# Kernel optimization log

Hardware: AMD Instinct MI355X
Metric: run time of the kernel (lower is better)

The kernel has to match this reference:

```python
import jax, jax.numpy as jnp
import numpy as np

B, S, D, F, E, K = 4, 2048, 512, 2048, 8, 2


def setup_inputs() -> dict:
    key = jax.random.key(0)
    kx, kg, kw, kv, k2 = jax.random.split(key, 5)
    scale = 0.02
    return {
        "x": jax.random.normal(kx, (B, S, D), dtype=jnp.float32),
        "Wg": jax.random.normal(kg, (D, E), dtype=jnp.float32) * scale,
        "W": jax.random.normal(kw, (E, D, F), dtype=jnp.float32) * scale,
        "V": jax.random.normal(kv, (E, D, F), dtype=jnp.float32) * scale,
        "W2": jax.random.normal(k2, (E, F, D), dtype=jnp.float32) * scale,
    }


def reference(x, Wg, W, V, W2):
    # Gating: top-k over expert logits, softmax over the selected k logits.
    gate_logits = jnp.einsum("bsd,de->bse", x, Wg)                 # [B,S,E]
    topv, topi = jax.lax.top_k(gate_logits, K)                      # [B,S,K]
    w = jax.nn.softmax(topv, axis=-1)                               # [B,S,K]
    # Dense per-token combine weights: gw[b,s,e] = sum_k w[b,s,k]*[topi[b,s,k]==e]
    gw = jnp.sum(w[..., None] * jax.nn.one_hot(topi, E, dtype=x.dtype), axis=-2)  # [B,S,E]

    y = jnp.zeros_like(x)
    n_experts = W.shape[0]
    for e in range(n_experts):  # fixed small loop over experts
        h = jax.nn.silu(jnp.einsum("bsd,df->bsf", x, W[e])) * jnp.einsum("bsd,df->bsf", x, V[e])
        y = y + gw[..., e:e + 1] * jnp.einsum("bsf,fd->bsd", h, W2[e])
    return y
```

## Files before the change

### kernel.cpp

```cpp
#include <hip/hip_runtime.h>
#include <hip/hip_bf16.h>
#include <stdint.h>

#define TT 8192
#define DD 512
#define FF 2048
#define EE 8
#define MAXT 136

typedef __attribute__((ext_vector_type(8))) short bf16x8;
typedef __attribute__((ext_vector_type(4))) float f32x4;

static __device__ __forceinline__ unsigned short f2b(float f) {
  union { __hip_bfloat16 b; unsigned short u; } cv;
  cv.b = __float2bfloat16(f);
  return cv.u;
}

static __device__ __forceinline__ void gload16(const void* g, void* l) {
  __builtin_amdgcn_global_load_lds(
      (const __attribute__((address_space(1))) unsigned int*)g,
      (__attribute__((address_space(3))) unsigned int*)l, 16, 0, 0);
}

#define VMCNT12 asm volatile("s_waitcnt vmcnt(12)" ::: "memory")
#define VMCNT6  asm volatile("s_waitcnt vmcnt(6)" ::: "memory")
#define VMCNT0  asm volatile("s_waitcnt vmcnt(0)" ::: "memory")
#define BARX    asm volatile("s_barrier" ::: "memory")

__launch_bounds__(256)
__global__ void k_prep(const float* __restrict__ x, const float* __restrict__ Wg,
                       unsigned short* __restrict__ xb,
                       int* __restrict__ te, float* __restrict__ tw) {
  int wid = threadIdx.x >> 6, lane = threadIdx.x & 63;
  int t = blockIdx.x * 4 + wid;
  const float* xr = x + (size_t)t * DD;
  unsigned short* xbr = xb + (size_t)t * DD;
  int d0 = lane * 8;

  float4 v0 = *(const float4*)(xr + d0);
  float4 v1 = *(const float4*)(xr + d0 + 4);
  ushort4 o0, o1;
  o0.x = f2b(v0.x); o0.y = f2b(v0.y); o0.z = f2b(v0.z); o0.w = f2b(v0.w);
  o1.x = f2b(v1.x); o1.y = f2b(v1.y); o1.z = f2b(v1.z); o1.w = f2b(v1.w);
  *(ushort4*)(xbr + d0) = o0;
  *(ushort4*)(xbr + d0 + 4) = o1;

  float xv[8] = {v0.x, v0.y, v0.z, v0.w, v1.x, v1.y, v1.z, v1.w};
  float acc[EE];
#pragma unroll
  for (int e = 0; e < EE; e++) acc[e] = 0.f;
#pragma unroll
  for (int j = 0; j < 8; j++) {
    const float* wg = Wg + (size_t)(d0 + j) * EE;
    float4 a = *(const float4*)wg;
    float4 b = *(const float4*)(wg + 4);
    acc[0] += xv[j] * a.x; acc[1] += xv[j] * a.y; acc[2] += xv[j] * a.z; acc[3] += xv[j] * a.w;
    acc[4] += xv[j] * b.x; acc[5] += xv[j] * b.y; acc[6] += xv[j] * b.z; acc[7] += xv[j] * b.w;
  }
#pragma unroll
  for (int e = 0; e < EE; e++)
    for (int o = 32; o; o >>= 1) acc[e] += __shfl_xor(acc[e], o);
  if (lane == 0) {
    int e1 = 0; float v1m = acc[0];
#pragma unroll
    for (int e = 1; e < EE; e++) if (acc[e] > v1m) { v1m = acc[e]; e1 = e; }
    int e2 = -1; float v2m = -INFINITY;
#pragma unroll
    for (int e = 0; e < EE; e++) if (e != e1 && acc[e] > v2m) { v2m = acc[e]; e2 = e; }
    float ex = __expf(v2m - v1m);
    float w1 = 1.f / (1.f + ex);
    float w2 = ex / (1.f + ex);
    te[t * 2] = e1; te[t * 2 + 1] = e2;
    tw[t * 2] = w1; tw[t * 2 + 1] = w2;
  }
}

__global__ void k_tcvt_all(const float* __restrict__ W, const float* __restrict__ V,
                           const float* __restrict__ W2, unsigned short* __restrict__ Wt,
                           unsigned short* __restrict__ Vt, unsigned short* __restrict__ W2t) {
  __shared__ float tile[32][33];
  int z = blockIdx.y;
  const float* src; unsigned short* dst; int N, nbx;
  if (z < 16) {
    int e = z & 7;
    size_t base = (size_t)e * DD * FF;
    src = (z < 8 ? W : V) + base;
    dst = (z < 8 ? Wt : Vt) + base;
    N = FF; nbx = FF / 32;
  } else {
    int e = z - 16;
    size_t base = (size_t)e * DD * FF;
    src = W2 + base; dst = W2t + base;
    N = DD; nbx = DD / 32;
  }
  int M = (z < 16) ? DD : FF;
  int bx = blockIdx.x;
  int cb = (bx % nbx) * 32, rb = (bx / nbx) * 32;
  int tx = threadIdx.x, ty = threadIdx.y;
#pragma unroll
  for (int i = 0; i < 4; i++)
    tile[ty + i * 8][tx] = src[(size_t)(rb + ty + i * 8) * N + cb + tx];
  __syncthreads();
#pragma unroll
  for (int i = 0; i < 4; i++)
    dst[(size_t)(cb + ty + i * 8) * M + rb + tx] = f2b(tile[tx][ty + i * 8]);
}

__launch_bounds__(1024)
__global__ void k_route(const int* __restrict__ te, const float* __restrict__ tw,
                        int* __restrict__ ctrl, int* __restrict__ perm,
                        float* __restrict__ pw, int* __restrict__ tileE,
                        int* __restrict__ tileRow, int* __restrict__ inv) {
  __shared__ int wsum[17][EE];
  __shared__ int ebase[EE];
  int tid = threadIdx.x;
  int lane = tid & 63, wid = tid >> 6;
  int myte[16]; float mytw[16];
  int c[EE];
#pragma unroll
  for (int e = 0; e < EE; e++) c[e] = 0;
  int s0 = tid * 16;
#pragma unroll
  for (int j = 0; j < 16; j++) {
    myte[j] = te[s0 + j];
    mytw[j] = tw[s0 + j];
#pragma unroll
    for (int e = 0; e < EE; e++) if (myte[j] == e) c[e]++;
  }
  int incl[EE];
#pragma unroll
  for (int e = 0; e < EE; e++) incl[e] = c[e];
  for (int off = 1; off < 64; off <<= 1) {
#pragma unroll
    for (int e = 0; e < EE; e++) {
      int v = __shfl_up(incl[e], off);
      if (lane >= off) incl[e] += v;
    }
  }
  if (lane == 63)
#pragma unroll
    for (int e = 0; e < EE; e++) wsum[wid][e] = incl[e];
  __syncthreads();
  if (tid < EE) {
    int s = 0;
    for (int w = 0; w < 16; w++) { int v = wsum[w][tid]; wsum[w][tid] = s; s += v; }
    wsum[16][tid] = s;
  }
  __syncthreads();
  if (tid == 0) {
    int s = 0, nt = 0;
    for (int e = 0; e < EE; e++) {
      int cnt = wsum[16][e];
      ebase[e] = s; ctrl[8 + e] = s; ctrl[e] = cnt;
      for (int i = 0; i < cnt; i += 128) { tileE[nt] = e; tileRow[nt] = s + i; nt++; }
      s += cnt;
    }
    ctrl[16] = s; ctrl[17] = nt;
  }
  __syncthreads();
#pragma unroll
  for (int e = 0; e < EE; e++) {
    int p = ebase[e] + wsum[wid][e] + incl[e] - c[e];
#pragma unroll
    for (int j = 0; j < 16; j++) {
      if (myte[j] == e) {
        perm[p] = (s0 + j) >> 1;
        pw[p] = mytw[j];
        inv[s0 + j] = p;
        p++;
      }
    }
  }
}

__launch_bounds__(256, 2)
__global__ void k_ffn1(const unsigned short* __restrict__ xb,
                       const unsigned short* __restrict__ Wt,
                       const unsigned short* __restrict__ Vt,
                       const int* __restrict__ perm, const float* __restrict__ pw,
                       const int* __restrict__ ctrl, const int* __restrict__ tileE,
                       const int* __restrict__ tileRow,
                       unsigned short* __restrict__ h) {
  int ti = blockIdx.y;
  if (ti >= ctrl[17]) return;
  int e = tileE[ti];
  int row0 = tileRow[ti];
  int last = ctrl[8 + e] + ctrl[e] - 1;
  int f0 = blockIdx.x * 128;

  __shared__ __align__(16) short As[3][128 * 32];
  __shared__ __align__(16) short Bs[3][256 * 32];

  int tid = threadIdx.x;
  int lane = tid & 63, wid = tid >> 6;
  int wr = wid >> 1, wc = wid & 1;

  int sl = (((tid & 3) ^ ((tid >> 3) & 3))) * 8;

  int ar1 = row0 + (tid >> 2); if (ar1 > last) ar1 = last;
  int ar2 = row0 + (tid >> 2) + 64; if (ar2 > last) ar2 = last;
  const unsigned short* agp1 = xb + (size_t)perm[ar1] * DD + sl;
  const unsigned short* agp2 = xb + (size_t)perm[ar2] * DD + sl;
  const unsigned short* wgp1 = Wt + ((size_t)e * FF + f0 + (tid >> 2)) * DD + sl;
  const unsigned short* wgp2 = wgp1 + (size_t)64 * DD;
  const unsigned short* vgp1 = Vt + ((size_t)e * FF + f0 + (tid >> 2)) * DD + sl;
  const unsigned short* vgp2 = vgp1 + (size_t)64 * DD;

#define STAGE1(buf, k0) do { \
    gload16(agp1 + (k0), &As[buf][tid * 8]); \
    gload16(agp2 + (k0), &As[buf][(tid + 256) * 8]); \
    gload16(wgp1 + (k0), &Bs[buf][tid * 8]); \
    gload16(wgp2 + (k0), &Bs[buf][(tid + 256) * 8]); \
    gload16(vgp1 + (k0), &Bs[buf][(tid + 512) * 8]); \
    gload16(vgp2 + (k0), &Bs[buf][(tid + 768) * 8]); \
  } while (0)

  f32x4 zz = {0.f, 0.f, 0.f, 0.f};
  f32x4 accw[4][4], accv[4][4];
#pragma unroll
  for (int m = 0; m < 4; m++)
#pragma unroll
    for (int n = 0; n < 4; n++) { accw[m][n] = zz; accv[m][n] = zz; }

  int lrow = lane & 15;
  int jx = (((lane >> 4) ^ ((lane >> 1) & 3))) * 8;

#define COMP1(buf) do { \
    bf16x8 a[4], bw[4], bv[4]; \
    _Pragma("unroll") \
    for (int m = 0; m < 4; m++) a[m] = *(bf16x8*)&As[buf][(wr * 64 + m * 16 + lrow) * 32 + jx]; \
    _Pragma("unroll") \
    for (int n = 0; n < 4; n++) { \
      bw[n] = *(bf16x8*)&Bs[buf][(wc * 64 + n * 16 + lrow) * 32 + jx]; \
      bv[n] = *(bf16x8*)&Bs[buf][(128 + wc * 64 + n * 16 + lrow) * 32 + jx]; \
    } \
    _Pragma("unroll") \
    for (int m = 0; m < 4; m++) \
      _Pragma("unroll") \
      for (int n = 0; n < 4; n++) { \
        accw[m][n] = __builtin_amdgcn_mfma_f32_16x16x32_bf16(a[m], bw[n], accw[m][n], 0, 0, 0); \
        accv[m][n] = __builtin_amdgcn_mfma_f32_16x16x32_bf16(a[m], bv[n], accv[m][n], 0, 0, 0); \
      } \
  } while (0)

  STAGE1(0, 0); STAGE1(1, 32); STAGE1(2, 64);
#pragma unroll 1
  for (int kt = 0; kt < 4; kt++) {
    VMCNT12; BARX; COMP1(0); BARX; STAGE1(0, (kt * 3 + 3) * 32);
    VMCNT12; BARX; COMP1(1); BARX; STAGE1(1, (kt * 3 + 4) * 32);
    VMCNT12; BARX; COMP1(2); BARX; STAGE1(2, (kt * 3 + 5) * 32);
  }
  VMCNT12; BARX; COMP1(0); BARX; STAGE1(0, 15 * 32);
  VMCNT12; BARX; COMP1(1);
  VMCNT6;  BARX; COMP1(2);
  VMCNT0;  BARX; COMP1(0);
#undef STAGE1
#undef COMP1

#pragma unroll
  for (int m = 0; m < 4; m++) {
    int rbase = row0 + wr * 64 + m * 16 + (lane >> 4) * 4;
#pragma unroll
    for (int reg = 0; reg < 4; reg++) {
      int r = rbase + reg;
      if (r > last) continue;
      float pwv = pw[r];
      size_t hrow = (size_t)r * FF;
#pragma unroll
      for (int n = 0; n < 4; n++) {
        float a = accw[m][n][reg];
        float b = accv[m][n][reg];
        float hv = a / (1.f + __expf(-a)) * b * pwv;
        h[hrow + f0 + wc * 64 + n * 16 + lrow] = f2b(hv);
      }
    }
  }
}

__launch_bounds__(256)
__global__ void k_ffn2(const unsigned short* __restrict__ h,
                       const unsigned short* __restrict__ W2t,
                       const int* __restrict__ ctrl,
                       const int* __restrict__ tileE, const int* __restrict__ tileRow,
                       float* __restrict__ yp) {
  int ti = blockIdx.y;
  if (ti >= ctrl[17]) return;
  int e = tileE[ti];
  int row0 = tileRow[ti];
  int last = ctrl[8 + e] + ctrl[e] - 1;
  int d0 = blockIdx.x * 128;

  __shared__ __align__(16) short As[2][128 * 32];
  __shared__ __align__(16) short Bs[2][128 * 32];

  int tid = threadIdx.x;
  int lane = tid & 63, wid = tid >> 6;
  int wm = (wid >> 1) * 64, wn = (wid & 1) * 64;

  int sl = (((tid & 3) ^ ((tid >> 3) & 3))) * 8;

  int ar1 = row0 + (tid >> 2); if (ar1 > last) ar1 = last;
  int ar2 = row0 + (tid >> 2) + 64; if (ar2 > last) ar2 = last;
  const unsigned short* agp1 = h + (size_t)ar1 * FF + sl;
  const unsigned short* agp2 = h + (size_t)ar2 * FF + sl;
  const unsigned short* bgp1 = W2t + ((size_t)e * DD + d0 + (tid >> 2)) * FF + sl;
  const unsigned short* bgp2 = bgp1 + (size_t)64 * FF;

#define STAGE2(buf, k0) do { \
    gload16(agp1 + (k0), &As[buf][tid * 8]); \
    gload16(agp2 + (k0), &As[buf][(tid + 256) * 8]); \
    gload16(bgp1 + (k0), &Bs[buf][tid * 8]); \
    gload16(bgp2 + (k0), &Bs[buf][(tid + 256) * 8]); \
  } while (0)

  f32x4 zz = {0.f, 0.f, 0.f, 0.f};
  f32x4 acc[4][4];
#pragma unroll
  for (int m = 0; m < 4; m++)
#pragma unroll
    for (int n = 0; n < 4; n++) acc[m][n] = zz;

  int lrow = lane & 15;
  int jx = (((lane >> 4) ^ ((lane >> 1) & 3))) * 8;

#define COMP2(buf) do { \
    bf16x8 a[4], b[4]; \
    _Pragma("unroll") \
    for (int m = 0; m < 4; m++) a[m] = *(bf16x8*)&As[buf][(wm + m * 16 + lrow) * 32 + jx]; \
    _Pragma("unroll") \
    for (int n = 0; n < 4; n++) b[n] = *(bf16x8*)&Bs[buf][(wn + n * 16 + lrow) * 32 + jx]; \
    _Pragma("unroll") \
    for (int m = 0; m < 4; m++) \
      _Pragma("unroll") \
      for (int n = 0; n < 4; n++) \
        acc[m][n] = __builtin_amdgcn_mfma_f32_16x16x32_bf16(a[m], b[n], acc[m][n], 0, 0, 0); \
  } while (0)

  STAGE2(0, 0);
  __syncthreads();
#pragma unroll 1
  for (int ks = 0; ks < 64; ks += 2) {
    if (ks + 1 < 64) STAGE2(1, (ks + 1) * 32);
    COMP2(0);
    __syncthreads();
    if (ks + 2 < 64) STAGE2(0, (ks + 2) * 32);
    COMP2(1);
    __syncthreads();
  }
#undef STAGE2
#undef COMP2

#pragma unroll
  for (int m = 0; m < 4; m++) {
    int rbase = row0 + wm + m * 16 + (lane >> 4) * 4;
#pragma unroll
    for (int reg = 0; reg < 4; reg++) {
      int r = rbase + reg;
      if (r > last) continue;
      float* ypr = yp + (size_t)r * DD + d0;
#pragma unroll
      for (int n = 0; n < 4; n++)
        ypr[wn + n * 16 + lrow] = acc[m][n][reg];
    }
  }
}

__launch_bounds__(256)
__global__ void k_gather(const float4* __restrict__ yp4, const int* __restrict__ inv,
                         float4* __restrict__ y4) {
  int i = blockIdx.x * 256 + threadIdx.x;
  int t = i >> 7, c = i & 127;
  int pa = inv[2 * t], pb = inv[2 * t + 1];
  float4 a = yp4[(size_t)pa * 128 + c];
  float4 b = yp4[(size_t)pb * 128 + c];
  float4 o;
  o.x = a.x + b.x; o.y = a.y + b.y; o.z = a.z + b.z; o.w = a.w + b.w;
  y4[i] = o;
}

extern "C" void kernel_launch(void* const* d_in, const int* in_sizes, int n_in,
                              void* d_out, int out_size, void* d_ws, size_t ws_size,
                              hipStream_t stream) {
  const float* x  = (const float*)d_in[0];
  const float* Wg = (const float*)d_in[1];
  const float* W  = (const float*)d_in[2];
  const float* V  = (const float*)d_in[3];
  const float* W2 = (const float*)d_in[4];
  float* y = (float*)d_out;

  char* ws = (char*)d_ws;
  size_t off = 0;
  auto alloc = [&](size_t n) -> char* {
    char* p = ws + off;
    off += (n + 255) & ~(size_t)255;
    return p;
  };
  unsigned short* xb  = (unsigned short*)alloc((size_t)TT * DD * 2);
  unsigned short* Wt  = (unsigned short*)alloc((size_t)EE * DD * FF * 2);
  unsigned short* Vt  = (unsigned short*)alloc((size_t)EE * DD * FF * 2);
  unsigned short* W2t = (unsigned short*)alloc((size_t)EE * DD * FF * 2);
  unsigned short* h   = (unsigned short*)alloc((size_t)TT * 2 * FF * 2);
  int*   perm = (int*)alloc(TT * 2 * 4);
  float* pw   = (float*)alloc(TT * 2 * 4);
  int*   te   = (int*)alloc(TT * 2 * 4);
  float* tw   = (float*)alloc(TT * 2 * 4);
  int*   inv  = (int*)alloc(TT * 2 * 4);
  int*   ctrl = (int*)alloc(256);
  int*   tileE   = (int*)alloc(MAXT * 4);
  int*   tileRow = (int*)alloc(MAXT * 4);
  if (off > ws_size) return;

  float* yp = (float*)Wt;

  k_prep<<<TT / 4, 256, 0, stream>>>(x, Wg, xb, te, tw);
  k_tcvt_all<<<dim3(1024, 24), dim3(32, 8), 0, stream>>>(W, V, W2, Wt, Vt, W2t);
  k_route<<<1, 1024, 0, stream>>>(te, tw, ctrl, perm, pw, tileE, tileRow, inv);
  k_ffn1<<<dim3(FF / 128, MAXT), 256, 0, stream>>>(xb, Wt, Vt, perm, pw, ctrl, tileE, tileRow, h);
  k_ffn2<<<dim3(DD / 128, MAXT), 256, 0, stream>>>(h, W2t, ctrl, tileE, tileRow, yp);
  k_gather<<<TT * 128 / 256, 256, 0, stream>>>((const float4*)yp, inv, (float4*)y);
}
```

Measured before the change: 240.2 us.

## Remap FFN block indices for per-XCD weight reuse and triple-buffer ffn2

Both FFN kernels now use a 1D grid whose block index is decoded so that blocks with the same low three bits, which are dispatched round-robin to the same XCD, always work on the same weight column slice across many token tiles. The goal is for each XCD's L2 to keep reusing one slice of the expert weights instead of every XCD streaming all of them. ffn2 also moves from two LDS buffers with __syncthreads to three buffers, driven by explicit vmcnt waits and raw barriers, so global loads run further ahead of the MFMA work. This adds LDS use in ffn2 and hand-counted waits that must stay exactly matched to the load schedule.

Measured after the change: 251.9 us. 4.9% more time.

```diff
diff --git a/kernel.cpp b/kernel.cpp
--- a/kernel.cpp
+++ b/kernel.cpp
@@ -24,7 +24,9 @@
 }
 
 #define VMCNT12 asm volatile("s_waitcnt vmcnt(12)" ::: "memory")
+#define VMCNT8  asm volatile("s_waitcnt vmcnt(8)" ::: "memory")
 #define VMCNT6  asm volatile("s_waitcnt vmcnt(6)" ::: "memory")
+#define VMCNT4  asm volatile("s_waitcnt vmcnt(4)" ::: "memory")
 #define VMCNT0  asm volatile("s_waitcnt vmcnt(0)" ::: "memory")
 #define BARX    asm volatile("s_barrier" ::: "memory")
 
@@ -182,12 +184,16 @@
                        const int* __restrict__ ctrl, const int* __restrict__ tileE,
                        const int* __restrict__ tileRow,
                        unsigned short* __restrict__ h) {
-  int ti = blockIdx.y;
+  int b = blockIdx.x;
+  int idx = b >> 3;
+  int half = (idx >= MAXT) ? 1 : 0;
+  int ti = idx - MAXT * half;
+  int ftile = (b & 7) + 8 * half;
   if (ti >= ctrl[17]) return;
   int e = tileE[ti];
   int row0 = tileRow[ti];
   int last = ctrl[8 + e] + ctrl[e] - 1;
-  int f0 = blockIdx.x * 128;
+  int f0 = ftile * 128;
 
   __shared__ __align__(16) short As[3][128 * 32];
   __shared__ __align__(16) short Bs[3][256 * 32];
@@ -284,15 +290,17 @@
                        const int* __restrict__ ctrl,
                        const int* __restrict__ tileE, const int* __restrict__ tileRow,
                        float* __restrict__ yp) {
-  int ti = blockIdx.y;
+  int b = blockIdx.x;
+  int dt = (b & 7) & 3;
+  int ti = (b >> 3) + 68 * ((b & 7) >> 2);
   if (ti >= ctrl[17]) return;
   int e = tileE[ti];
   int row0 = tileRow[ti];
   int last = ctrl[8 + e] + ctrl[e] - 1;
-  int d0 = blockIdx.x * 128;
-
-  __shared__ __align__(16) short As[2][128 * 32];
-  __shared__ __align__(16) short Bs[2][128 * 32];
+  int d0 = dt * 128;
+
+  __shared__ __align__(16) short As[3][128 * 32];
+  __shared__ __align__(16) short Bs[3][128 * 32];
 
   int tid = threadIdx.x;
   int lane = tid & 63, wid = tid >> 6;
@@ -325,29 +333,29 @@
   int jx = (((lane >> 4) ^ ((lane >> 1) & 3))) * 8;
 
 #define COMP2(buf) do { \
-    bf16x8 a[4], b[4]; \
+    bf16x8 a[4], bb[4]; \
     _Pragma("unroll") \
     for (int m = 0; m < 4; m++) a[m] = *(bf16x8*)&As[buf][(wm + m * 16 + lrow) * 32 + jx]; \
     _Pragma("unroll") \
-    for (int n = 0; n < 4; n++) b[n] = *(bf16x8*)&Bs[buf][(wn + n * 16 + lrow) * 32 + jx]; \
+    for (int n = 0; n < 4; n++) bb[n] = *(bf16x8*)&Bs[buf][(wn + n * 16 + lrow) * 32 + jx]; \
     _Pragma("unroll") \
     for (int m = 0; m < 4; m++) \
       _Pragma("unroll") \
       for (int n = 0; n < 4; n++) \
-        acc[m][n] = __builtin_amdgcn_mfma_f32_16x16x32_bf16(a[m], b[n], acc[m][n], 0, 0, 0); \
+        acc[m][n] = __builtin_amdgcn_mfma_f32_16x16x32_bf16(a[m], bb[n], acc[m][n], 0, 0, 0); \
   } while (0)
 
-  STAGE2(0, 0);
-  __syncthreads();
+  STAGE2(0, 0); STAGE2(1, 32); STAGE2(2, 64);
 #pragma unroll 1
-  for (int ks = 0; ks < 64; ks += 2) {
-    if (ks + 1 < 64) STAGE2(1, (ks + 1) * 32);
-    COMP2(0);
-    __syncthreads();
-    if (ks + 2 < 64) STAGE2(0, (ks + 2) * 32);
-    COMP2(1);
-    __syncthreads();
-  }
+  for (int kt = 0; kt < 20; kt++) {
+    VMCNT8; BARX; COMP2(0); BARX; STAGE2(0, (kt * 3 + 3) * 32);
+    VMCNT8; BARX; COMP2(1); BARX; STAGE2(1, (kt * 3 + 4) * 32);
+    VMCNT8; BARX; COMP2(2); BARX; STAGE2(2, (kt * 3 + 5) * 32);
+  }
+  VMCNT8; BARX; COMP2(0); BARX; STAGE2(0, 63 * 32);
+  VMCNT8; BARX; COMP2(1);
+  VMCNT4; BARX; COMP2(2);
+  VMCNT0; BARX; COMP2(0);
 #undef STAGE2
 #undef COMP2
 
@@ -416,7 +424,7 @@
   k_prep<<<TT / 4, 256, 0, stream>>>(x, Wg, xb, te, tw);
   k_tcvt_all<<<dim3(1024, 24), dim3(32, 8), 0, stream>>>(W, V, W2, Wt, Vt, W2t);
   k_route<<<1, 1024, 0, stream>>>(te, tw, ctrl, perm, pw, tileE, tileRow, inv);
-  k_ffn1<<<dim3(FF / 128, MAXT), 256, 0, stream>>>(xb, Wt, Vt, perm, pw, ctrl, tileE, tileRow, h);
-  k_ffn2<<<dim3(DD / 128, MAXT), 256, 0, stream>>>(h, W2t, ctrl, tileE, tileRow, yp);
+  k_ffn1<<<16 * MAXT, 256, 0, stream>>>(xb, Wt, Vt, perm, pw, ctrl, tileE, tileRow, h);
+  k_ffn2<<<4 * MAXT, 256, 0, stream>>>(h, W2t, ctrl, tileE, tileRow, yp);
   k_gather<<<TT * 128 / 256, 256, 0, stream>>>((const float4*)yp, inv, (float4*)y);
 }
```
